# Kernel tuning notes

Hardware: AMD Instinct MI355X
Metric: run time of the kernel (lower is better)

Reference implementation:

```python
import jax, jax.numpy as jnp
import numpy as np

SOFTENING = 0.01
SOFTENING_SQ = SOFTENING * SOFTENING


def setup_inputs() -> dict:
    key = jax.random.key(0)
    k1, k2 = jax.random.split(key)
    N = 8192
    positions = jax.random.normal(k1, (N, 3), dtype=jnp.float32)
    masses = jax.random.uniform(k2, (N,), dtype=jnp.float32)
    return {"positions": positions, "masses": masses}


def reference(positions, masses):
    # diff[i, j] = r_j - r_i  -> shape (N, N, 3)
    diff = positions[None, :, :] - positions[:, None, :]
    dist_sq = jnp.sum(diff * diff, axis=2) + SOFTENING_SQ        # (N, N)
    inv_dist_cubed = dist_sq ** (-1.5)                            # (N, N)
    # a_i = sum_j m_j * diff[i, j] * inv_dist_cubed[i, j]
    w = masses[None, :] * inv_dist_cubed                          # (N, N)
    accelerations = jnp.einsum('ij,ijd->id', w, diff)             # (N, 3)
    return accelerations
```

## Files before the change

### kernel.cpp

```cpp
#include <hip/hip_runtime.h>

#define NBODY 8192
#define BLOCK 256
#define SLABS 32
#define JCHUNK (NBODY / SLABS)
#define SOFT2 1.0e-4f

__global__ __launch_bounds__(BLOCK) void nbody_kernel(
    const float* __restrict__ pos, const float* __restrict__ mass,
    float* __restrict__ out) {
  __shared__ float4 tile[JCHUNK];

  const int t = threadIdx.x;
  const int i = blockIdx.x * BLOCK + t;
  const int j0 = blockIdx.y * JCHUNK;

  const int j = j0 + t;
  tile[t] = make_float4(pos[j * 3 + 0], pos[j * 3 + 1], pos[j * 3 + 2],
                        mass[j]);

  const float xi = pos[i * 3 + 0];
  const float yi = pos[i * 3 + 1];
  const float zi = pos[i * 3 + 2];

  __syncthreads();

  float ax = 0.f, ay = 0.f, az = 0.f;
#pragma unroll 8
  for (int k = 0; k < JCHUNK; ++k) {
    float4 o = tile[k];
    float dx = o.x - xi;
    float dy = o.y - yi;
    float dz = o.z - zi;
    float r2 = fmaf(dx, dx, fmaf(dy, dy, fmaf(dz, dz, SOFT2)));
    float inv = __builtin_amdgcn_rsqf(r2);
    float w = o.w * (inv * inv * inv);
    ax = fmaf(w, dx, ax);
    ay = fmaf(w, dy, ay);
    az = fmaf(w, dz, az);
  }

  atomicAdd(&out[i * 3 + 0], ax);
  atomicAdd(&out[i * 3 + 1], ay);
  atomicAdd(&out[i * 3 + 2], az);
}

extern "C" void kernel_launch(void* const* d_in, const int* in_sizes, int n_in,
                              void* d_out, int out_size, void* d_ws,
                              size_t ws_size, hipStream_t stream) {
  const float* pos = (const float*)d_in[0];
  const float* mass = (const float*)d_in[1];
  float* out = (float*)d_out;

  hipMemsetAsync(d_out, 0, (size_t)out_size * sizeof(float), stream);

  dim3 grid(NBODY / BLOCK, SLABS);
  nbody_kernel<<<grid, BLOCK, 0, stream>>>(pos, mass, out);
}
```

Before: 78.66 us.

## Use packed FP32 math with 4 bodies per thread and deterministic two-pass reduction

Each thread now handles four target bodies, using two-wide packed float vectors so the compiler can emit packed FP32 instructions, and each j-tile load from LDS is reused across four bodies. The j-dimension split rises to 128 slabs of 64 bodies. Atomics and the memset are replaced by per-slab partial outputs in workspace plus a separate reduction kernel. This adds a second launch and about 12 MB of partial-sum traffic, and the four-body accumulator state raises register pressure.

```diff
diff --git a/kernel.cpp b/kernel.cpp
--- a/kernel.cpp
+++ b/kernel.cpp
@@ -1,48 +1,105 @@
 #include <hip/hip_runtime.h>
+
+typedef float v2f __attribute__((ext_vector_type(2)));
 
 #define NBODY 8192
 #define BLOCK 256
-#define SLABS 32
+#define IPT 4
+#define ITILE (BLOCK * IPT)
+#define NITILES (NBODY / ITILE)
+#define SLABS 128
 #define JCHUNK (NBODY / SLABS)
+#define NF (NBODY * 3)
 #define SOFT2 1.0e-4f
 
-__global__ __launch_bounds__(BLOCK) void nbody_kernel(
+static __device__ __forceinline__ v2f splat(float s) { return (v2f){s, s}; }
+
+__global__ __launch_bounds__(BLOCK) void force_kernel(
     const float* __restrict__ pos, const float* __restrict__ mass,
-    float* __restrict__ out) {
+    float* __restrict__ part) {
   __shared__ float4 tile[JCHUNK];
 
   const int t = threadIdx.x;
-  const int i = blockIdx.x * BLOCK + t;
   const int j0 = blockIdx.y * JCHUNK;
+  if (t < JCHUNK) {
+    const int j = j0 + t;
+    tile[t] =
+        make_float4(pos[j * 3 + 0], pos[j * 3 + 1], pos[j * 3 + 2], mass[j]);
+  }
 
-  const int j = j0 + t;
-  tile[t] = make_float4(pos[j * 3 + 0], pos[j * 3 + 1], pos[j * 3 + 2],
-                        mass[j]);
+  const int ib = blockIdx.x * ITILE + t;
+  float xs[4], ys[4], zs[4];
+#pragma unroll
+  for (int p = 0; p < 4; ++p) {
+    const int i = ib + p * BLOCK;
+    xs[p] = pos[i * 3 + 0];
+    ys[p] = pos[i * 3 + 1];
+    zs[p] = pos[i * 3 + 2];
+  }
+  const v2f xA = {xs[0], xs[1]}, xB = {xs[2], xs[3]};
+  const v2f yA = {ys[0], ys[1]}, yB = {ys[2], ys[3]};
+  const v2f zA = {zs[0], zs[1]}, zB = {zs[2], zs[3]};
 
-  const float xi = pos[i * 3 + 0];
-  const float yi = pos[i * 3 + 1];
-  const float zi = pos[i * 3 + 2];
+  v2f axA = {0.f, 0.f}, ayA = {0.f, 0.f}, azA = {0.f, 0.f};
+  v2f axB = {0.f, 0.f}, ayB = {0.f, 0.f}, azB = {0.f, 0.f};
 
   __syncthreads();
 
-  float ax = 0.f, ay = 0.f, az = 0.f;
-#pragma unroll 8
+#pragma unroll 4
   for (int k = 0; k < JCHUNK; ++k) {
-    float4 o = tile[k];
-    float dx = o.x - xi;
-    float dy = o.y - yi;
-    float dz = o.z - zi;
-    float r2 = fmaf(dx, dx, fmaf(dy, dy, fmaf(dz, dz, SOFT2)));
-    float inv = __builtin_amdgcn_rsqf(r2);
-    float w = o.w * (inv * inv * inv);
-    ax = fmaf(w, dx, ax);
-    ay = fmaf(w, dy, ay);
-    az = fmaf(w, dz, az);
+    const float4 o = tile[k];
+    const v2f ox = splat(o.x), oy = splat(o.y), oz = splat(o.z);
+    const v2f om = splat(o.w);
+
+    v2f dxA = ox - xA, dyA = oy - yA, dzA = oz - zA;
+    v2f dxB = ox - xB, dyB = oy - yB, dzB = oz - zB;
+    v2f r2A = dxA * dxA + (dyA * dyA + (dzA * dzA + splat(SOFT2)));
+    v2f r2B = dxB * dxB + (dyB * dyB + (dzB * dzB + splat(SOFT2)));
+
+    const float iA0 = __builtin_amdgcn_rsqf(r2A.x);
+    const float iA1 = __builtin_amdgcn_rsqf(r2A.y);
+    const float iB0 = __builtin_amdgcn_rsqf(r2B.x);
+    const float iB1 = __builtin_amdgcn_rsqf(r2B.y);
+    const v2f iA = {iA0, iA1}, iB = {iB0, iB1};
+
+    v2f wA = ((iA * iA) * iA) * om;
+    v2f wB = ((iB * iB) * iB) * om;
+
+    axA += wA * dxA;
+    ayA += wA * dyA;
+    azA += wA * dzA;
+    axB += wB * dxB;
+    ayB += wB * dyB;
+    azB += wB * dzB;
   }
 
-  atomicAdd(&out[i * 3 + 0], ax);
-  atomicAdd(&out[i * 3 + 1], ay);
-  atomicAdd(&out[i * 3 + 2], az);
+  float* __restrict__ dst = part + (size_t)blockIdx.y * NF;
+  const float ax[4] = {axA.x, axA.y, axB.x, axB.y};
+  const float ay[4] = {ayA.x, ayA.y, ayB.x, ayB.y};
+  const float az[4] = {azA.x, azA.y, azB.x, azB.y};
+#pragma unroll
+  for (int p = 0; p < 4; ++p) {
+    const int i = ib + p * BLOCK;
+    dst[0 * NBODY + i] = ax[p];
+    dst[1 * NBODY + i] = ay[p];
+    dst[2 * NBODY + i] = az[p];
+  }
+}
+
+__global__ __launch_bounds__(BLOCK) void reduce_kernel(
+    const float* __restrict__ part, float* __restrict__ out) {
+  const int idx = blockIdx.x * BLOCK + threadIdx.x;
+  const int c = idx >> 13;
+  const int b = idx & (NBODY - 1);
+  float s0 = 0.f, s1 = 0.f, s2 = 0.f, s3 = 0.f;
+#pragma unroll 8
+  for (int sl = 0; sl < SLABS; sl += 4) {
+    s0 += part[(size_t)(sl + 0) * NF + idx];
+    s1 += part[(size_t)(sl + 1) * NF + idx];
+    s2 += part[(size_t)(sl + 2) * NF + idx];
+    s3 += part[(size_t)(sl + 3) * NF + idx];
+  }
+  out[b * 3 + c] = (s0 + s1) + (s2 + s3);
 }
 
 extern "C" void kernel_launch(void* const* d_in, const int* in_sizes, int n_in,
@@ -51,9 +108,8 @@
   const float* pos = (const float*)d_in[0];
   const float* mass = (const float*)d_in[1];
   float* out = (float*)d_out;
+  float* part = (float*)d_ws;
 
-  hipMemsetAsync(d_out, 0, (size_t)out_size * sizeof(float), stream);
-
-  dim3 grid(NBODY / BLOCK, SLABS);
-  nbody_kernel<<<grid, BLOCK, 0, stream>>>(pos, mass, out);
+  force_kernel<<<dim3(NITILES, SLABS), BLOCK, 0, stream>>>(pos, mass, part);
+  reduce_kernel<<<NF / BLOCK, BLOCK, 0, stream>>>(part, out);
 }
```

Result: slower. 85.57 us (+8.8%).
